# Kernel tuning notes

Hardware: AMD Instinct MI355X
Metric: run time of the kernel (lower is better)

Reference implementation:

```python
import jax, jax.numpy as jnp
import numpy as np

B, V, M, H, T = 512, 256, 128, 512, 16  # batch, vocab, memory_size, hidden_dim, timing_dim
ALPHA = 0.95


def setup_inputs() -> dict:
    key = jax.random.key(0)
    ks = jax.random.split(key, 8)
    return {
        "x": jax.random.uniform(ks[0], (B, V), dtype=jnp.float32),
        "memory": jax.random.normal(ks[1], (B, M, V), dtype=jnp.float32),
        "memory_timings": jax.random.randint(ks[2], (B, M), 0, 1000, dtype=jnp.int64) if jax.config.jax_enable_x64 else jax.random.randint(ks[2], (B, M), 0, 1000).astype(jnp.int32),
        "memory_surprise": jax.random.uniform(ks[3], (B, M), dtype=jnp.float32),
        "last_prediction": jax.random.uniform(ks[4], (B, V), dtype=jnp.float32),
        "W1": jax.random.normal(ks[5], (V * M + M * T, H), dtype=jnp.float32) * 0.01,
        "b1": jnp.zeros((H,), dtype=jnp.float32),
        "W2": jax.random.normal(ks[6], (H, V), dtype=jnp.float32) * 0.01,
        "b2": jnp.zeros((V,), dtype=jnp.float32),
    }


def reference(x, memory, memory_timings, memory_surprise, last_prediction, W1, b1, W2, b2):
    b = x.shape[0]
    ar = jnp.arange(b)
    # compute_surprise
    surprise = -jnp.sum(x * jnp.log(last_prediction + 1e-6), axis=1)  # [B]
    # update_memory_timings
    timings = memory_timings + 1
    msurp = memory_surprise * ALPHA
    # update_memory: argmin-scatter into memory/timings/surprise
    idx = jnp.argmin(msurp, axis=1)  # [B]
    memory = memory.at[ar, idx].set(x)
    timings = timings.at[ar, idx].set(0)
    msurp = msurp.at[ar, idx].set(surprise)
    # compute_prediction: sort by timing, gather-reorder memory
    order = jnp.argsort(timings, axis=1)  # stable ascending, [B, M]
    sorted_t = jnp.take_along_axis(timings, order, axis=1)  # [B, M]
    sorted_mem = jnp.take_along_axis(memory, order[:, :, None], axis=1)  # [B, M, V]
    # binary encoding of timings: (t // 2**k) % 2 for k in [0, T)
    bits = ((sorted_t[:, :, None] >> jnp.arange(T)) & 1).astype(jnp.float32)  # [B, M, T]
    pred_in = jnp.concatenate([sorted_mem.reshape(b, -1), bits.reshape(b, -1)], axis=1)
    h = jax.nn.relu(pred_in @ W1 + b1)
    return h @ W2 + b2
```

## Files before the change

kernel.cpp:

```cpp
#include <hip/hip_runtime.h>

typedef unsigned int uint;
typedef unsigned short ushort;
typedef __attribute__((ext_vector_type(8))) short short8;
typedef __attribute__((ext_vector_type(4))) float f32x4;

#define B_   512
#define V_   256
#define M_   128
#define H_   512
#define T_   16
#define KTOT 34816

__device__ __forceinline__ ushort f2bf(float f) {
  uint u = __builtin_bit_cast(uint, f);
  u += 0x7fffu + ((u >> 16) & 1u);
  return (ushort)(u >> 16);
}
__device__ __forceinline__ float bf2f(ushort s) {
  return __builtin_bit_cast(float, ((uint)s) << 16);
}

__device__ __forceinline__ int swz_k(int k, int row) {
  return (k & ~31) | (((((k >> 3) & 3) ^ ((row >> 1) & 3)) << 3)) | (k & 7);
}

__global__ __launch_bounds__(256) void prep_kernel(
    const float* __restrict__ x, const float* __restrict__ mem,
    const int* __restrict__ timings, const float* __restrict__ msurp,
    const float* __restrict__ b1,
    ushort* __restrict__ A, float* __restrict__ h_pre)
{
  const int b = blockIdx.x, tid = threadIdx.x;
  __shared__ int s_t[M_];
  __shared__ int s_row[M_];
  __shared__ int s_st[M_];
  __shared__ int s_idx;

  if (tid < 64) {
    float v0 = msurp[b * M_ + tid];
    float v1 = msurp[b * M_ + tid + 64];
    float v; int i;
    if (v1 < v0) { v = v1; i = tid + 64; } else { v = v0; i = tid; }
    #pragma unroll
    for (int off = 32; off > 0; off >>= 1) {
      float ov = __shfl_down(v, off);
      int   oi = __shfl_down(i, off);
      if (ov < v || (ov == v && oi < i)) { v = ov; i = oi; }
    }
    if (tid == 0) s_idx = i;
  }
  __syncthreads();
  const int idx = s_idx;

  if (tid < M_) {
    int t = timings[b * M_ + tid] + 1;
    if (tid == idx) t = 0;
    s_t[tid] = t;
  }
  h_pre[(size_t)b * H_ + tid]       = b1[tid];
  h_pre[(size_t)b * H_ + 256 + tid] = b1[256 + tid];
  __syncthreads();

  if (tid < M_) {
    const int t = s_t[tid];
    int r = 0;
    for (int j = 0; j < M_; ++j) {
      int tj = s_t[j];
      r += (tj < t || (tj == t && j < tid)) ? 1 : 0;
    }
    s_row[r] = tid;
    s_st[r]  = t;
  }
  __syncthreads();

  if (tid < M_) {
    const int t = s_st[tid];
    uint p[8];
    #pragma unroll
    for (int h = 0; h < 8; ++h) {
      uint lo = ((t >> (2 * h)) & 1) ? 0x3F80u : 0u;
      uint hi = ((t >> (2 * h + 1)) & 1) ? 0x3F80u : 0u;
      p[h] = lo | (hi << 16);
    }
    const int k0 = V_ * M_ + tid * T_;
    uint4 w0; w0.x = p[0]; w0.y = p[1]; w0.z = p[2]; w0.w = p[3];
    uint4 w1; w1.x = p[4]; w1.y = p[5]; w1.z = p[6]; w1.w = p[7];
    *(uint4*)(A + (size_t)b * KTOT + swz_k(k0, b))     = w0;
    *(uint4*)(A + (size_t)b * KTOT + swz_k(k0 + 8, b)) = w1;
  }

  const int lane = tid & 63, sub = tid >> 6;
  for (int it = 0; it < 32; ++it) {
    const int slot = it * 4 + sub;
    const int rowm = s_row[slot];
    const float* src = (rowm == idx) ? (x + (size_t)b * V_)
                                     : (mem + ((size_t)b * M_ + rowm) * V_);
    f32x4 v = *(const f32x4*)(src + lane * 4);
    uint2 o;
    o.x = (uint)f2bf(v[0]) | ((uint)f2bf(v[1]) << 16);
    o.y = (uint)f2bf(v[2]) | ((uint)f2bf(v[3]) << 16);
    const int k = slot * V_ + lane * 4;
    *(uint2*)(A + (size_t)b * KTOT + swz_k(k, b)) = o;
  }
}

#define BM 256
#define BN 128
#define SPLITK 64
#define KCH 544
#define NCHU 17

#define GLD16(g, l) __builtin_amdgcn_global_load_lds( \
  (const __attribute__((address_space(1))) void*)(g), \
  (__attribute__((address_space(3))) void*)(l), 16, 0, 0)

template<bool USE_ATOMIC>
__global__ __launch_bounds__(512, 4) void gemm1_kernel(
    const ushort* __restrict__ A, const float* __restrict__ W1,
    void* __restrict__ dstv)
{
  __shared__ __align__(16) ushort As[3][BM * 32];
  __shared__ __align__(16) ushort Bs[2][BN * 32];

  const int bid  = blockIdx.x;
  const int sk   = (bid & 7) | ((bid >> 6) << 3);
  const int tile = (bid >> 3) & 7;
  const int b0   = (tile >> 2) * BM;
  const int n0   = (tile & 3) * BN;
  const int tid  = threadIdx.x, wave = tid >> 6, lane = tid & 63;
  const int wm   = wave >> 1;
  const int wn   = wave & 1;
  const long kb0 = (long)sk * KCH;

  f32x4 acc[4][4];
  #pragma unroll
  for (int i = 0; i < 4; ++i)
    #pragma unroll
    for (int j = 0; j < 4; ++j) acc[i][j] = (f32x4)0.f;

  const int ar  = wave * 32 + (lane >> 2);
  const int akk = (lane & 3) * 8;
  auto stageA = [&](int buf, int chunk) {
    const long kb = kb0 + (long)chunk * 32;
    GLD16(A + ((size_t)(b0 + ar))      * KTOT + kb + akk, &As[buf][(wave * 32) * 32]);
    GLD16(A + ((size_t)(b0 + ar + 16)) * KTOT + kb + akk, &As[buf][(wave * 32 + 16) * 32]);
  };

  const int bn_  = tid & 127;
  const int bkc  = tid >> 7;
  const float* w1p = W1 + (size_t)(kb0 + bkc * 8) * H_ + n0 + bn_;
  const int b_woff = bn_ * 32 + ((bkc ^ ((bn_ >> 1) & 3)) * 8);

  auto loadB = [&](float* r, int c) {
    const float* p = w1p + (size_t)c * 32 * H_;
    #pragma unroll
    for (int i = 0; i < 8; ++i) r[i] = p[(size_t)i * H_];
  };
  auto writeB = [&](const float* r, ushort* d) {
    uint4 o;
    o.x = (uint)f2bf(r[0]) | ((uint)f2bf(r[1]) << 16);
    o.y = (uint)f2bf(r[2]) | ((uint)f2bf(r[3]) << 16);
    o.z = (uint)f2bf(r[4]) | ((uint)f2bf(r[5]) << 16);
    o.w = (uint)f2bf(r[6]) | ((uint)f2bf(r[7]) << 16);
    *(uint4*)d = o;
  };

  const int xo     = (((lane >> 4) ^ ((lane >> 1) & 3)) * 8);
  const int a_roff = (wm * 64 + (lane & 15)) * 32;
  const int b_roff = (wn * 64 + (lane & 15)) * 32;

  float brE[8], brO[8];

#define GITER(c, BRL, BRW, ISSUE, WRITE, VMC) do {                            \
    asm volatile("s_waitcnt vmcnt(" VMC ") lgkmcnt(0)" ::: "memory");         \
    __builtin_amdgcn_s_barrier();                                             \
    __builtin_amdgcn_sched_barrier(0);                                        \
    if (ISSUE) { loadB(BRL, (c) + 2); stageA(((c) + 2) % 3, (c) + 2); }       \
    const ushort* as_ = &As[(c) % 3][a_roff + xo];                            \
    const ushort* bs_ = &Bs[(c) & 1][b_roff + xo];                            \
    short8 af[4], bf[4];                                                      \
    _Pragma("unroll") for (int i = 0; i < 4; ++i) {                           \
      af[i] = *(const short8*)(as_ + i * 16 * 32);                            \
      bf[i] = *(const short8*)(bs_ + i * 16 * 32); }                          \
    _Pragma("unroll") for (int i = 0; i < 4; ++i)                             \
      _Pragma("unroll") for (int j = 0; j < 4; ++j)                           \
        acc[i][j] = __builtin_amdgcn_mfma_f32_16x16x32_bf16(af[i], bf[j],     \
                                                            acc[i][j], 0,0,0);\
    if (WRITE) writeB(BRW, &Bs[((c) + 1) & 1][b_woff]);                       \
  } while (0)

  loadB(brE, 0);
  stageA(0, 0);
  loadB(brO, 1);
  stageA(1, 1);
  writeB(brE, &Bs[0][b_woff]);

  #pragma unroll 1
  for (int cc = 0; cc < 14; cc += 2) {
    GITER(cc,     brE, brO, true, true, "10");
    GITER(cc + 1, brO, brE, true, true, "10");
  }
  GITER(14, brE, brO, true,  true,  "10");
  GITER(15, brO, brE, false, true,  "10");
  GITER(16, brE, brO, false, false, "0");
#undef GITER

  const int row0 = b0 + wm * 64 + (lane >> 4) * 4;
  const int col0 = n0 + wn * 64 + (lane & 15);
  if constexpr (USE_ATOMIC) {
    float* dst = (float*)dstv;
    #pragma unroll
    for (int i = 0; i < 4; ++i)
      #pragma unroll
      for (int j = 0; j < 4; ++j)
        #pragma unroll
        for (int r = 0; r < 4; ++r)
          atomicAdd(&dst[(size_t)(row0 + i * 16 + r) * H_ + col0 + j * 16], acc[i][j][r]);
  } else {
    ushort* P = (ushort*)dstv + (size_t)sk * (B_ * H_);
    #pragma unroll
    for (int i = 0; i < 4; ++i)
      #pragma unroll
      for (int j = 0; j < 4; ++j)
        #pragma unroll
        for (int r = 0; r < 4; ++r)
          P[(size_t)(row0 + i * 16 + r) * H_ + col0 + j * 16] = f2bf(acc[i][j][r]);
  }
}

template<bool FROM_PARTIALS>
__global__ __launch_bounds__(256) void gemm2_kernel(
    const void* __restrict__ Pin, const float* __restrict__ b1,
    const float* __restrict__ W2, const float* __restrict__ b2,
    float* __restrict__ out)
{
  const int bb = blockIdx.x * 2;
  const int v  = threadIdx.x;
  __shared__ float hs[2][H_];

  {
    const int id  = v * 4;
    const int row = id >> 9, col = id & 511;
    f32x4 s;
    if constexpr (FROM_PARTIALS) {
      const ushort* P = (const ushort*)Pin;
      s = *(const f32x4*)(b1 + col);
      #pragma unroll 4
      for (int sk = 0; sk < SPLITK; ++sk) {
        uint2 u = *(const uint2*)(P + (size_t)sk * (B_ * H_) + (size_t)(bb + row) * H_ + col);
        s[0] += bf2f((ushort)(u.x & 0xffff));
        s[1] += bf2f((ushort)(u.x >> 16));
        s[2] += bf2f((ushort)(u.y & 0xffff));
        s[3] += bf2f((ushort)(u.y >> 16));
      }
    } else {
      s = *(const f32x4*)((const float*)Pin + (size_t)(bb + row) * H_ + col);
    }
    f32x4 r;
    #pragma unroll
    for (int t = 0; t < 4; ++t) r[t] = fmaxf(s[t], 0.f);
    *(f32x4*)&hs[row][col] = r;
  }
  __syncthreads();

  float a0 = 0.f, a1 = 0.f;
  for (int j4 = 0; j4 < H_ / 4; ++j4) {
    f32x4 h0 = *(const f32x4*)&hs[0][j4 * 4];
    f32x4 h1 = *(const f32x4*)&hs[1][j4 * 4];
    #pragma unroll
    for (int t = 0; t < 4; ++t) {
      float w = W2[(size_t)(j4 * 4 + t) * V_ + v];
      a0 += h0[t] * w; a1 += h1[t] * w;
    }
  }
  const float bias = b2[v];
  out[(size_t)(bb + 0) * V_ + v] = a0 + bias;
  out[(size_t)(bb + 1) * V_ + v] = a1 + bias;
}

extern "C" void kernel_launch(void* const* d_in, const int* in_sizes, int n_in,
                              void* d_out, int out_size, void* d_ws, size_t ws_size,
                              hipStream_t stream) {
  const float* x   = (const float*)d_in[0];
  const float* mem = (const float*)d_in[1];
  const int*   tim = (const int*)d_in[2];
  const float* msu = (const float*)d_in[3];
  const float* W1  = (const float*)d_in[5];
  const float* b1  = (const float*)d_in[6];
  const float* W2  = (const float*)d_in[7];
  const float* b2  = (const float*)d_in[8];
  float* out = (float*)d_out;

  char* ws = (char*)d_ws;
  const size_t abytes = (size_t)B_ * KTOT * 2;
  const size_t pbytes = (size_t)SPLITK * B_ * H_ * 2;
  const size_t hbytes = (size_t)B_ * H_ * 4;
  const bool partials = ws_size >= abytes + pbytes + hbytes;

  ushort* A_ws  = (ushort*)ws;
  void*   P     = (void*)(ws + abytes);
  float*  h_pre = partials ? (float*)(ws + abytes + pbytes)
                           : (float*)(ws + abytes);

  prep_kernel<<<B_, 256, 0, stream>>>(x, mem, tim, msu, b1, A_ws, h_pre);
  if (partials) {
    gemm1_kernel<false><<<8 * SPLITK, 512, 0, stream>>>(A_ws, W1, P);
    gemm2_kernel<true><<<B_ / 2, 256, 0, stream>>>(P, b1, W2, b2, out);
  } else {
    gemm1_kernel<true><<<8 * SPLITK, 512, 0, stream>>>(A_ws, W1, h_pre);
    gemm2_kernel<false><<<B_ / 2, 256, 0, stream>>>(h_pre, b1, W2, b2, out);
  }
}
```

Measured before the change: 76.26 us.

## Widen gemm1 N-tile to 256 so each A chunk feeds more MFMAs

Doubles the gemm1 output tile width from 128 to 256 columns. Each block now runs a 4x8 MFMA accumulator grid per wave, loads 16 W1 rows per thread, and the grid shrinks to 4*SPLITK blocks. The aim is to halve redundant A-tile global loads and increase MFMA work per staged chunk. In exchange it doubles accumulator registers, lowers the occupancy target to 2, and launches only 256 blocks, which may underfill the GPU.

```diff
diff --git a/kernel.cpp b/kernel.cpp
--- a/kernel.cpp
+++ b/kernel.cpp
@@ -106,7 +106,7 @@
 }
 
 #define BM 256
-#define BN 128
+#define BN 256
 #define SPLITK 64
 #define KCH 544
 #define NCHU 17
@@ -116,7 +116,7 @@
   (__attribute__((address_space(3))) void*)(l), 16, 0, 0)
 
 template<bool USE_ATOMIC>
-__global__ __launch_bounds__(512, 4) void gemm1_kernel(
+__global__ __launch_bounds__(512, 2) void gemm1_kernel(
     const ushort* __restrict__ A, const float* __restrict__ W1,
     void* __restrict__ dstv)
 {
@@ -124,20 +124,20 @@
   __shared__ __align__(16) ushort Bs[2][BN * 32];
 
   const int bid  = blockIdx.x;
-  const int sk   = (bid & 7) | ((bid >> 6) << 3);
-  const int tile = (bid >> 3) & 7;
-  const int b0   = (tile >> 2) * BM;
-  const int n0   = (tile & 3) * BN;
+  const int sk   = (bid & 7) | ((bid >> 5) << 3);
+  const int tile = (bid >> 3) & 3;
+  const int b0   = (tile >> 1) * BM;
+  const int n0   = (tile & 1) * BN;
   const int tid  = threadIdx.x, wave = tid >> 6, lane = tid & 63;
   const int wm   = wave >> 1;
   const int wn   = wave & 1;
   const long kb0 = (long)sk * KCH;
 
-  f32x4 acc[4][4];
+  f32x4 acc[4][8];
   #pragma unroll
   for (int i = 0; i < 4; ++i)
     #pragma unroll
-    for (int j = 0; j < 4; ++j) acc[i][j] = (f32x4)0.f;
+    for (int j = 0; j < 8; ++j) acc[i][j] = (f32x4)0.f;
 
   const int ar  = wave * 32 + (lane >> 2);
   const int akk = (lane & 3) * 8;
@@ -147,73 +147,89 @@
     GLD16(A + ((size_t)(b0 + ar + 16)) * KTOT + kb + akk, &As[buf][(wave * 32 + 16) * 32]);
   };
 
-  const int bn_  = tid & 127;
-  const int bkc  = tid >> 7;
-  const float* w1p = W1 + (size_t)(kb0 + bkc * 8) * H_ + n0 + bn_;
-  const int b_woff = bn_ * 32 + ((bkc ^ ((bn_ >> 1) & 3)) * 8);
+  const int ncol = tid & 255;
+  const int kh   = tid >> 8;
+  const float* w1p = W1 + (size_t)(kb0 + kh * 16) * H_ + n0 + ncol;
+  const int sg   = (ncol >> 1) & 3;
+  const int kc0  = kh * 2;
+  const int bw0  = ncol * 32 + ((kc0 ^ sg) * 8);
+  const int bw1  = ncol * 32 + (((kc0 + 1) ^ sg) * 8);
 
   auto loadB = [&](float* r, int c) {
     const float* p = w1p + (size_t)c * 32 * H_;
     #pragma unroll
-    for (int i = 0; i < 8; ++i) r[i] = p[(size_t)i * H_];
+    for (int i = 0; i < 16; ++i) r[i] = p[(size_t)i * H_];
   };
-  auto writeB = [&](const float* r, ushort* d) {
-    uint4 o;
-    o.x = (uint)f2bf(r[0]) | ((uint)f2bf(r[1]) << 16);
-    o.y = (uint)f2bf(r[2]) | ((uint)f2bf(r[3]) << 16);
-    o.z = (uint)f2bf(r[4]) | ((uint)f2bf(r[5]) << 16);
-    o.w = (uint)f2bf(r[6]) | ((uint)f2bf(r[7]) << 16);
-    *(uint4*)d = o;
+  auto writeB = [&](const float* r, ushort* base) {
+    uint4 o0, o1;
+    o0.x = (uint)f2bf(r[0])  | ((uint)f2bf(r[1])  << 16);
+    o0.y = (uint)f2bf(r[2])  | ((uint)f2bf(r[3])  << 16);
+    o0.z = (uint)f2bf(r[4])  | ((uint)f2bf(r[5])  << 16);
+    o0.w = (uint)f2bf(r[6])  | ((uint)f2bf(r[7])  << 16);
+    o1.x = (uint)f2bf(r[8])  | ((uint)f2bf(r[9])  << 16);
+    o1.y = (uint)f2bf(r[10]) | ((uint)f2bf(r[11]) << 16);
+    o1.z = (uint)f2bf(r[12]) | ((uint)f2bf(r[13]) << 16);
+    o1.w = (uint)f2bf(r[14]) | ((uint)f2bf(r[15]) << 16);
+    *(uint4*)(base + bw0) = o0;
+    *(uint4*)(base + bw1) = o1;
   };
 
   const int xo     = (((lane >> 4) ^ ((lane >> 1) & 3)) * 8);
   const int a_roff = (wm * 64 + (lane & 15)) * 32;
-  const int b_roff = (wn * 64 + (lane & 15)) * 32;
-
-  float brE[8], brO[8];
+  const int b_roff = (wn * 128 + (lane & 15)) * 32;
+
+  float brE[16], brO[16];
 
 #define GITER(c, BRL, BRW, ISSUE, WRITE, VMC) do {                            \
     asm volatile("s_waitcnt vmcnt(" VMC ") lgkmcnt(0)" ::: "memory");         \
     __builtin_amdgcn_s_barrier();                                             \
     __builtin_amdgcn_sched_barrier(0);                                        \
-    if (ISSUE) { loadB(BRL, (c) + 2); stageA(((c) + 2) % 3, (c) + 2); }       \
+    if (ISSUE) { stageA(((c) + 2) % 3, (c) + 2); loadB(BRL, (c) + 2); }       \
     const ushort* as_ = &As[(c) % 3][a_roff + xo];                            \
     const ushort* bs_ = &Bs[(c) & 1][b_roff + xo];                            \
     short8 af[4], bf[4];                                                      \
-    _Pragma("unroll") for (int i = 0; i < 4; ++i) {                           \
+    _Pragma("unroll") for (int i = 0; i < 4; ++i)                             \
       af[i] = *(const short8*)(as_ + i * 16 * 32);                            \
-      bf[i] = *(const short8*)(bs_ + i * 16 * 32); }                          \
+    _Pragma("unroll") for (int j = 0; j < 4; ++j)                             \
+      bf[j] = *(const short8*)(bs_ + j * 16 * 32);                            \
     _Pragma("unroll") for (int i = 0; i < 4; ++i)                             \
       _Pragma("unroll") for (int j = 0; j < 4; ++j)                           \
         acc[i][j] = __builtin_amdgcn_mfma_f32_16x16x32_bf16(af[i], bf[j],     \
                                                             acc[i][j], 0,0,0);\
-    if (WRITE) writeB(BRW, &Bs[((c) + 1) & 1][b_woff]);                       \
+    _Pragma("unroll") for (int j = 0; j < 4; ++j)                             \
+      bf[j] = *(const short8*)(bs_ + (j + 4) * 16 * 32);                      \
+    _Pragma("unroll") for (int i = 0; i < 4; ++i)                             \
+      _Pragma("unroll") for (int j = 0; j < 4; ++j)                           \
+        acc[i][j + 4] = __builtin_amdgcn_mfma_f32_16x16x32_bf16(af[i], bf[j], \
+                                                            acc[i][j + 4],    \
+                                                            0, 0, 0);         \
+    if (WRITE) writeB(BRW, &Bs[((c) + 1) & 1][0]);                            \
   } while (0)
 
+  stageA(0, 0);
   loadB(brE, 0);
-  stageA(0, 0);
+  stageA(1, 1);
   loadB(brO, 1);
-  stageA(1, 1);
-  writeB(brE, &Bs[0][b_woff]);
+  writeB(brE, &Bs[0][0]);
 
   #pragma unroll 1
   for (int cc = 0; cc < 14; cc += 2) {
-    GITER(cc,     brE, brO, true, true, "10");
-    GITER(cc + 1, brO, brE, true, true, "10");
-  }
-  GITER(14, brE, brO, true,  true,  "10");
-  GITER(15, brO, brE, false, true,  "10");
+    GITER(cc,     brE, brO, true, true, "18");
+    GITER(cc + 1, brO, brE, true, true, "18");
+  }
+  GITER(14, brE, brO, true,  true,  "18");
+  GITER(15, brO, brE, false, true,  "18");
   GITER(16, brE, brO, false, false, "0");
 #undef GITER
 
   const int row0 = b0 + wm * 64 + (lane >> 4) * 4;
-  const int col0 = n0 + wn * 64 + (lane & 15);
+  const int col0 = n0 + wn * 128 + (lane & 15);
   if constexpr (USE_ATOMIC) {
     float* dst = (float*)dstv;
     #pragma unroll
     for (int i = 0; i < 4; ++i)
       #pragma unroll
-      for (int j = 0; j < 4; ++j)
+      for (int j = 0; j < 8; ++j)
         #pragma unroll
         for (int r = 0; r < 4; ++r)
           atomicAdd(&dst[(size_t)(row0 + i * 16 + r) * H_ + col0 + j * 16], acc[i][j][r]);
@@ -222,7 +238,7 @@
     #pragma unroll
     for (int i = 0; i < 4; ++i)
       #pragma unroll
-      for (int j = 0; j < 4; ++j)
+      for (int j = 0; j < 8; ++j)
         #pragma unroll
         for (int r = 0; r < 4; ++r)
           P[(size_t)(row0 + i * 16 + r) * H_ + col0 + j * 16] = f2bf(acc[i][j][r]);
@@ -305,10 +321,10 @@
 
   prep_kernel<<<B_, 256, 0, stream>>>(x, mem, tim, msu, b1, A_ws, h_pre);
   if (partials) {
-    gemm1_kernel<false><<<8 * SPLITK, 512, 0, stream>>>(A_ws, W1, P);
+    gemm1_kernel<false><<<4 * SPLITK, 512, 0, stream>>>(A_ws, W1, P);
     gemm2_kernel<true><<<B_ / 2, 256, 0, stream>>>(P, b1, W2, b2, out);
   } else {
-    gemm1_kernel<true><<<8 * SPLITK, 512, 0, stream>>>(A_ws, W1, h_pre);
+    gemm1_kernel<true><<<4 * SPLITK, 512, 0, stream>>>(A_ws, W1, h_pre);
     gemm2_kernel<false><<<B_ / 2, 256, 0, stream>>>(h_pre, b1, W2, b2, out);
   }
 }
```

Measured after the change: 75.02 us. No clear change (-1.6%).
